# Performance work log

Measured on AMD Instinct MI355X. Metric: run time of the kernel, lower is better.

Reference implementation:

```python
import jax, jax.numpy as jnp
import numpy as np

N, C, H, W = 4, 128, 64, 64
HEADS, KS, RED = 4, 7, 18
D = C // HEADS


def _layernorm(x, w, b, eps=1e-5):
    mu = x.mean(axis=-1, keepdims=True)
    var = ((x - mu) ** 2).mean(axis=-1, keepdims=True)
    return (x - mu) * jax.lax.rsqrt(var + eps) * w + b


def _gelu(x):
    return jax.nn.gelu(x, approximate=False)


def setup_inputs() -> dict:
    key = jax.random.key(0)
    ks = jax.random.split(key, 16)
    s = 0.02
    inp = {
        'x': jax.random.normal(ks[0], (N, C, H, W), jnp.float32),
        'ln1_w': jnp.ones((C,), jnp.float32), 'ln1_b': jnp.zeros((C,), jnp.float32),
        'ln2_w': jnp.ones((C,), jnp.float32), 'ln2_b': jnp.zeros((C,), jnp.float32),
        'qkv_w': jax.random.normal(ks[1], (C, 3 * C), jnp.float32) * s,
        'qkv_b': jnp.zeros((3 * C,), jnp.float32),
        'proj_w': jax.random.normal(ks[2], (C, C), jnp.float32) * s,
        'proj_b': jnp.zeros((C,), jnp.float32),
        'rpb': jax.random.normal(ks[3], (HEADS, 2 * KS - 1, 2 * KS - 1), jnp.float32) * s,
        'conv1_w': jax.random.normal(ks[4], (C, C // 4), jnp.float32) * s,
        'conv1_b': jnp.zeros((C // 4,), jnp.float32),
        'conv2_w': jax.random.normal(ks[5], (C // 4, C), jnp.float32) * s,
        'conv2_b': jnp.zeros((C,), jnp.float32),
        'ca1_w': jax.random.normal(ks[6], (C, C // RED), jnp.float32) * s,
        'ca1_b': jnp.zeros((C // RED,), jnp.float32),
        'ca2_w': jax.random.normal(ks[7], (C // RED, C), jnp.float32) * s,
        'ca2_b': jnp.zeros((C,), jnp.float32),
        'fc1_w': jax.random.normal(ks[8], (C, 4 * C), jnp.float32) * s,
        'fc1_b': jnp.zeros((4 * C,), jnp.float32),
        'fc2_w': jax.random.normal(ks[9], (4 * C, C), jnp.float32) * s,
        'fc2_b': jnp.zeros((C,), jnp.float32),
    }
    return inp


def _na2d(xc, qkv_w, qkv_b, rpb, proj_w, proj_b):
    # xc: [N, H, W, C] -> neighborhood attention with clamped k x k windows (NATTEN semantics)
    n, h, w, c = xc.shape
    qkv = (xc @ qkv_w + qkv_b).reshape(n, h, w, 3, HEADS, D)
    q, k, v = qkv[..., 0, :, :], qkv[..., 1, :, :], qkv[..., 2, :, :]
    q = q * (D ** -0.5)
    half = KS // 2
    ni = jnp.clip(jnp.arange(h) - half, 0, h - KS)          # window start per query row
    nj = jnp.clip(jnp.arange(w) - half, 0, w - KS)
    idx_i = ni[:, None] + jnp.arange(KS)                     # [H, KS]
    idx_j = nj[:, None] + jnp.arange(KS)                     # [W, KS]
    # gather key/value windows: [N, H, KS, W, KS, heads, D]
    kw = k[:, idx_i][:, :, :, idx_j]
    vw = v[:, idx_i][:, :, :, idx_j]
    attn = jnp.einsum('nijhd,niajbhd->nijhab', q, kw)        # [N,H,W,heads,KS,KS]
    bi = idx_i - jnp.arange(h)[:, None] + (KS - 1)           # rel-pos bias row index [H,KS]
    bj = idx_j - jnp.arange(w)[:, None] + (KS - 1)           # [W,KS]
    bias = rpb[:, bi][:, :, :, bj]                           # [heads,H,KS,W,KS]
    attn = attn + bias.transpose(1, 3, 0, 2, 4)[None]        # -> [1,H,W,heads,KS,KS]
    attn = jax.nn.softmax(attn.reshape(n, h, w, HEADS, KS * KS), axis=-1)
    attn = attn.reshape(n, h, w, HEADS, KS, KS)
    out = jnp.einsum('nijhab,niajbhd->nijhd', attn, vw).reshape(n, h, w, c)
    return out @ proj_w + proj_b


def reference(x, ln1_w, ln1_b, ln2_w, ln2_b, qkv_w, qkv_b, proj_w, proj_b, rpb,
              conv1_w, conv1_b, conv2_w, conv2_b, ca1_w, ca1_b, ca2_w, ca2_b,
              fc1_w, fc1_b, fc2_w, fc2_b):
    n, c, h, w = x.shape
    xs = x.transpose(0, 2, 3, 1).reshape(n, h * w, c)        # n (h w) c
    shortcut = xs
    xn = _layernorm(xs, ln1_w, ln1_b)
    xc = xn.reshape(n, h, w, c)
    # conv branch: 1x1 -> GELU -> 1x1 -> channel attention
    t = _gelu(xc @ conv1_w + conv1_b) @ conv2_w + conv2_b
    g = t.mean(axis=(1, 2))                                  # global avg pool [N,C]
    g = jax.nn.sigmoid(jax.nn.relu(g @ ca1_w + ca1_b) @ ca2_w + ca2_b)
    ca_x = (t * g[:, None, None, :]).reshape(n, h * w, c)
    # neighborhood attention branch
    na_x = _na2d(xc, qkv_w, qkv_b, rpb, proj_w, proj_b).reshape(n, h * w, c)
    x2 = shortcut + na_x + ca_x * 0.02
    m = _gelu(_layernorm(x2, ln2_w, ln2_b) @ fc1_w + fc1_b) @ fc2_w + fc2_b
    x3 = x2 + m
    return x3.reshape(n, h, w, c).transpose(0, 3, 1, 2)
```

## Files before the change

kernel.cpp:

```cpp
#include <hip/hip_runtime.h>
#include <hip/hip_bf16.h>
#include <math.h>

#define NB 4
#define CC 128
#define HH 64
#define WW 64
#define HEADS 4
#define KS 7
#define DD 32
#define HW 4096
#define MTOT 16384

typedef unsigned short BF;
typedef short short8 __attribute__((ext_vector_type(8)));
typedef float floatx4 __attribute__((ext_vector_type(4)));

__device__ __forceinline__ float gelu_f(float x) {
    return 0.5f * x * (1.0f + erff(x * 0.70710678118654752440f));
}

__device__ __forceinline__ BF f2bf(float f) {
    union { float f; unsigned u; } a; a.f = f;
    unsigned u = a.u;
    unsigned r = u + 0x7FFFu + ((u >> 16) & 1u);
    return (BF)(r >> 16);
}

__device__ __forceinline__ float bf2f(BF v) {
    return __uint_as_float(((unsigned)v) << 16);
}

#define LDK 40
#define LDK128 136

__global__ __launch_bounds__(256) void ln1t_kernel(
    const float* __restrict__ x, const float* __restrict__ w,
    const float* __restrict__ b, BF* __restrict__ out,
    float* __restrict__ part,
    const float* __restrict__ qkv_w, const float* __restrict__ conv1_w,
    const float* __restrict__ conv2_w, const float* __restrict__ proj_w,
    const float* __restrict__ fc1_w, const float* __restrict__ fc2_w,
    BF* __restrict__ qkvT, BF* __restrict__ c1T, BF* __restrict__ c2T,
    BF* __restrict__ projT2, BF* __restrict__ fc1T2, BF* __restrict__ fc2T2)
{
    const int blk = blockIdx.x;
    const int t  = threadIdx.x;

    if (blk >= 512) {
        for (int idx = (blk - 512) * 256 + t; idx < 204800; idx += 32768) {
            if (idx < 49152) {
                int l = idx, n = l >> 7, k = l & 127;
                qkvT[l] = f2bf(qkv_w[k * 384 + n]);
            } else if (idx < 53248) {
                int l = idx - 49152, n = l >> 7, k = l & 127;
                c1T[l] = f2bf(conv1_w[k * 32 + n]);
            } else if (idx < 57344) {
                int l = idx - 53248, n = l >> 5, k = l & 31;
                c2T[l] = f2bf(conv2_w[k * 128 + n]);
            } else if (idx < 73728) {
                int l = idx - 57344, kk = l & 31, n = (l >> 5) & 127, ks = l >> 12;
                projT2[l] = f2bf(proj_w[(ks * 32 + kk) * 128 + n]);
            } else if (idx < 139264) {
                int l = idx - 73728, kk = l & 31, n = (l >> 5) & 511, ks = l >> 14;
                fc1T2[l] = f2bf(fc1_w[(ks * 32 + kk) * 512 + n]);
            } else {
                int l = idx - 139264, kk = l & 31, n = (l >> 5) & 127, ks = l >> 12;
                fc2T2[l] = f2bf(fc2_w[(ks * 32 + kk) * 128 + n]);
            }
        }
        return;
    }

    __shared__ float xt[128][33];
    __shared__ float mus[32], rss[32];
    const int n  = blk >> 7;
    const int p0 = (blk & 127) * 32;
    if (blk < 4 && t < 128) part[blk * CC + t] = 0.f;

    {
        int pp = t & 31, c8 = t >> 5;
        #pragma unroll 4
        for (int it = 0; it < 16; it++) {
            int c = it * 8 + c8;
            xt[c][pp] = x[(size_t)(n * CC + c) * HW + p0 + pp];
        }
    }
    __syncthreads();
    {
        int pp2 = t >> 3, cb = t & 7;
        float s = 0.f;
        #pragma unroll
        for (int u = 0; u < 16; u++) s += xt[cb + u * 8][pp2];
        s += __shfl_xor(s, 1); s += __shfl_xor(s, 2); s += __shfl_xor(s, 4);
        float mu = s * (1.0f / CC);
        float v = 0.f;
        #pragma unroll
        for (int u = 0; u < 16; u++) { float d = xt[cb + u * 8][pp2] - mu; v += d * d; }
        v += __shfl_xor(v, 1); v += __shfl_xor(v, 2); v += __shfl_xor(v, 4);
        if (cb == 0) { mus[pp2] = mu; rss[pp2] = rsqrtf(v * (1.0f / CC) + 1e-5f); }
    }
    __syncthreads();
    {
        #pragma unroll
        for (int it = 0; it < 2; it++) {
            int pp2 = (t >> 4) + it * 16;
            int c0  = (t & 15) * 8;
            float mu = mus[pp2], rs = rss[pp2];
            int m = n * HW + p0 + pp2;
            short8 o;
            #pragma unroll
            for (int u = 0; u < 8; u++)
                o[u] = (short)f2bf((xt[c0 + u][pp2] - mu) * rs * w[c0 + u] + b[c0 + u]);
            *(short8*)(out + (size_t)m * CC + c0) = o;
        }
    }
}

__global__ __launch_bounds__(256) void phase2(
    const BF* __restrict__ xn, const BF* __restrict__ qkvT,
    const float* __restrict__ qkv_b, BF* __restrict__ qkv_out,
    const BF* __restrict__ c1T, const float* __restrict__ b1,
    const BF* __restrict__ c2T, const float* __restrict__ b2,
    BF* __restrict__ tout, float* __restrict__ part)
{
    __shared__ __align__(16) char smem[26624];
    const int bid = blockIdx.x;
    const int t = threadIdx.x;
    const int w = t >> 6, lane = t & 63, q = lane >> 4, r16 = lane & 15;

    if (bid < 768) {
        BF* Bl = (BF*)smem;
        const int col0 = (bid % 6) * 64;
        const int row0 = (bid / 6) * 128;
        {
            int nn = t >> 2;
            int kk = (t & 3) * 32;
            const BF* src = qkvT + (size_t)(col0 + nn) * 128 + kk;
            #pragma unroll
            for (int u = 0; u < 4; u++)
                *(uint4*)(Bl + nn * LDK128 + kk + u * 8) = *(const uint4*)(src + u * 8);
        }
        __syncthreads();
        #pragma unroll
        for (int half = 0; half < 2; half++) {
            floatx4 acc[4] = {};
            const BF* arow = xn + (size_t)(row0 + half * 64 + w * 16 + r16) * CC;
            #pragma unroll
            for (int ks = 0; ks < 4; ks++) {
                short8 af = *(const short8*)(arow + ks * 32 + q * 8);
                #pragma unroll
                for (int nt = 0; nt < 4; nt++) {
                    short8 bf = *(const short8*)(Bl + (nt * 16 + r16) * LDK128 + ks * 32 + q * 8);
                    acc[nt] = __builtin_amdgcn_mfma_f32_16x16x32_bf16(af, bf, acc[nt], 0, 0, 0);
                }
            }
            #pragma unroll
            for (int nt = 0; nt < 4; nt++) {
                int col = col0 + nt * 16 + r16;
                float bv = qkv_b[col];
                #pragma unroll
                for (int reg = 0; reg < 4; reg++) {
                    int row = row0 + half * 64 + w * 16 + q * 4 + reg;
                    qkv_out[(size_t)row * 384 + col] = f2bf(acc[nt][reg] + bv);
                }
            }
        }
        return;
    }
    BF*    W1l = (BF*)smem;
    BF*    W2l = (BF*)(smem + 8704);
    BF*    Hl  = (BF*)(smem + 18944);
    float* red = (float*)(smem + 24064);
    const int row0 = (bid - 768) * 64;
    {
        #pragma unroll
        for (int it = 0; it < 2; it++) {
            int idx = it * 256 + t;
            int nn = idx >> 4, u = idx & 15;
            *(uint4*)(W1l + nn * LDK128 + u * 8) = *(const uint4*)(c1T + nn * 128 + u * 8);
        }
    }
    {
        #pragma unroll
        for (int it = 0; it < 2; it++) {
            int idx = it * 256 + t;
            int nn = idx >> 2, u = idx & 3;
            *(uint4*)(W2l + nn * LDK + u * 8) = *(const uint4*)(c2T + nn * 32 + u * 8);
        }
    }
    __syncthreads();
    floatx4 a1[2] = {};
    const BF* arow = xn + (size_t)(row0 + w * 16 + r16) * CC;
    #pragma unroll
    for (int ks = 0; ks < 4; ks++) {
        short8 af = *(const short8*)(arow + ks * 32 + q * 8);
        #pragma unroll
        for (int nt = 0; nt < 2; nt++) {
            short8 bf = *(const short8*)(W1l + (nt * 16 + r16) * LDK128 + ks * 32 + q * 8);
            a1[nt] = __builtin_amdgcn_mfma_f32_16x16x32_bf16(af, bf, a1[nt], 0, 0, 0);
        }
    }
    #pragma unroll
    for (int nt = 0; nt < 2; nt++) {
        int col = nt * 16 + r16;
        float bv = b1[col];
        #pragma unroll
        for (int reg = 0; reg < 4; reg++)
            Hl[(w * 16 + q * 4 + reg) * LDK + col] = f2bf(gelu_f(a1[nt][reg] + bv));
    }
    __syncthreads();
    floatx4 a2[8] = {};
    short8 af2 = *(const short8*)(Hl + (w * 16 + r16) * LDK + q * 8);
    #pragma unroll
    for (int nt = 0; nt < 8; nt++) {
        short8 bf = *(const short8*)(W2l + (nt * 16 + r16) * LDK + q * 8);
        a2[nt] = __builtin_amdgcn_mfma_f32_16x16x32_bf16(af2, bf, a2[nt], 0, 0, 0);
    }
    #pragma unroll
    for (int nt = 0; nt < 8; nt++) {
        int col = nt * 16 + r16;
        float bv = b2[col];
        float s = 0.f;
        #pragma unroll
        for (int reg = 0; reg < 4; reg++) {
            int row = row0 + w * 16 + q * 4 + reg;
            float v = a2[nt][reg] + bv;
            tout[(size_t)row * CC + col] = f2bf(v);
            s += v;
        }
        s += __shfl_xor(s, 16);
        s += __shfl_xor(s, 32);
        if (lane < 16) red[w * 128 + col] = s;
    }
    __syncthreads();
    if (t < 128) {
        float cs = red[t] + red[128 + t] + red[256 + t] + red[384 + t];
        atomicAdd(&part[(row0 >> 12) * CC + t], cs);
    }
}

__global__ __launch_bounds__(256) void na_mfma_kernel(
    const BF* __restrict__ qkv, const float* __restrict__ rpb,
    BF* __restrict__ outp)
{
    __shared__ __align__(16) BF Kt[224][40];
    __shared__ __align__(16) BF Vt[32][232];
    __shared__ __align__(16) BF Qb[64][40];
    __shared__ __align__(16) BF Pl[4][16][232];
    __shared__ float rb[169];

    const int b = blockIdx.x;
    const int h = b & 3;
    const int tile = b >> 2;
    const int n = tile >> 6;
    const int ti = (tile >> 3) & 7, tj = tile & 7;
    const int t = threadIdx.x;
    const int w = t >> 6, lane = t & 63, quad = lane >> 4, r16 = lane & 15;
    const int i0 = ti * 8, j0 = tj * 8;
    const int wi0 = max(i0 - 3, 0), wj0 = max(j0 - 3, 0);
    const int R  = min(wi0 + 13, 63) - wi0 + 1;
    const int Rj = min(wj0 + 13, 63) - wj0 + 1;

    for (int idx = t; idx < 896; idx += 256) {
        int key = idx >> 2, ch = idx & 3;
        int kr = key >> 4, kc = key & 15;
        uint4 v = {0u, 0u, 0u, 0u};
        if (kr < R && kc < Rj) {
            size_t pix = (size_t)((n * HH + wi0 + kr) * WW + wj0 + kc);
            v = *(const uint4*)(qkv + pix * 384 + 128 + h * DD + ch * 8);
        }
        *(uint4*)&Kt[key][ch * 8] = v;
    }
    for (int idx = t; idx < 896; idx += 256) {
        int key = idx >> 2, ch = idx & 3;
        int kr = key >> 4, kc = key & 15;
        if (kr < R && kc < Rj) {
            size_t pix = (size_t)((n * HH + wi0 + kr) * WW + wj0 + kc);
            uint4 v = *(const uint4*)(qkv + pix * 384 + 256 + h * DD + ch * 8);
            const BF* pv = (const BF*)&v;
            #pragma unroll
            for (int u = 0; u < 8; u++) Vt[ch * 8 + u][key] = pv[u];
        } else {
            #pragma unroll
            for (int u = 0; u < 8; u++) Vt[ch * 8 + u][key] = 0;
        }
    }
    {
        int q = t >> 2, ch = t & 3;
        size_t mq = (size_t)((n * HH + i0 + (q >> 3)) * WW + j0 + (q & 7));
        *(uint4*)&Qb[q][ch * 8] = *(const uint4*)(qkv + mq * 384 + h * DD + ch * 8);
    }
    if (t < 169) rb[t] = rpb[h * 169 + t];
    __syncthreads();

    const int kt0 = min(max(i0 + 2 * w - 3, 0), HH - KS) - wi0;

    int oi[4], cok[4], bj0[4], ai_[4];
    #pragma unroll
    for (int reg = 0; reg < 4; reg++) {
        int q = w * 16 + quad * 4 + reg;
        int i = i0 + (q >> 3), j = j0 + (q & 7);
        int ni = min(max(i - 3, 0), HH - KS), nj = min(max(j - 3, 0), WW - KS);
        oi[reg]  = ni - wi0;
        ai_[reg] = ni - i + 6;
        int dc = r16 - (nj - wj0);
        cok[reg] = ((unsigned)dc < 7u) ? 1 : 0;
        bj0[reg] = min(max(dc + (nj - j + 6), 0), 12);
    }

    short8 aq = *(const short8*)&Qb[w * 16 + r16][quad * 8];
    floatx4 S[8];
    #pragma unroll
    for (int jt = 0; jt < 8; jt++) {
        floatx4 z = {0.f, 0.f, 0.f, 0.f};
        short8 bk = *(const short8*)&Kt[(kt0 + jt) * 16 + r16][quad * 8];
        S[jt] = __builtin_amdgcn_mfma_f32_16x16x32_bf16(aq, bk, z, 0, 0, 0);
    }
    const float scale = 0.17677669529663688110f;
    #pragma unroll
    for (int jt = 0; jt < 8; jt++) {
        #pragma unroll
        for (int reg = 0; reg < 4; reg++) {
            int dr = kt0 + jt - oi[reg];
            bool ok = ((unsigned)dr < 7u) && cok[reg];
            int bi = min(max(dr + ai_[reg], 0), 12);
            float bias = rb[bi * 13 + bj0[reg]];
            S[jt][reg] = ok ? fmaf(S[jt][reg], scale, bias) : -1e30f;
        }
    }
    float rinv[4];
    #pragma unroll
    for (int reg = 0; reg < 4; reg++) {
        float m = S[0][reg];
        #pragma unroll
        for (int jt = 1; jt < 8; jt++) m = fmaxf(m, S[jt][reg]);
        m = fmaxf(m, __shfl_xor(m, 1));
        m = fmaxf(m, __shfl_xor(m, 2));
        m = fmaxf(m, __shfl_xor(m, 4));
        m = fmaxf(m, __shfl_xor(m, 8));
        float s = 0.f;
        #pragma unroll
        for (int jt = 0; jt < 8; jt++) {
            float e = __expf(S[jt][reg] - m);
            S[jt][reg] = e;
            s += e;
        }
        s += __shfl_xor(s, 1);
        s += __shfl_xor(s, 2);
        s += __shfl_xor(s, 4);
        s += __shfl_xor(s, 8);
        rinv[reg] = 1.0f / s;
    }
    #pragma unroll
    for (int jt = 0; jt < 8; jt++)
        #pragma unroll
        for (int reg = 0; reg < 4; reg++)
            Pl[w][quad * 4 + reg][(kt0 + jt) * 16 + r16] = f2bf(S[jt][reg] * rinv[reg]);
    if (kt0 & 1) {
        #pragma unroll
        for (int reg = 0; reg < 4; reg++) {
            Pl[w][quad * 4 + reg][(kt0 - 1) * 16 + r16] = 0;
            Pl[w][quad * 4 + reg][(kt0 + 8) * 16 + r16] = 0;
        }
    }

    const int ks0 = kt0 >> 1;
    const int nch = 4 + (kt0 & 1);
    floatx4 O0 = {0.f, 0.f, 0.f, 0.f}, O1 = {0.f, 0.f, 0.f, 0.f};
    #pragma unroll
    for (int c2 = 0; c2 < 5; c2++) {
        if (c2 < nch) {
            int ks = ks0 + c2;
            short8 ap = *(const short8*)&Pl[w][r16][ks * 32 + quad * 8];
            short8 b0 = *(const short8*)&Vt[r16][ks * 32 + quad * 8];
            short8 b1 = *(const short8*)&Vt[16 + r16][ks * 32 + quad * 8];
            O0 = __builtin_amdgcn_mfma_f32_16x16x32_bf16(ap, b0, O0, 0, 0, 0);
            O1 = __builtin_amdgcn_mfma_f32_16x16x32_bf16(ap, b1, O1, 0, 0, 0);
        }
    }
    #pragma unroll
    for (int reg = 0; reg < 4; reg++) {
        int q = w * 16 + quad * 4 + reg;
        size_t m = (size_t)((n * HH + i0 + (q >> 3)) * WW + j0 + (q & 7));
        outp[m * CC + h * DD + r16]      = f2bf(O0[reg]);
        outp[m * CC + h * DD + 16 + r16] = f2bf(O1[reg]);
    }
}

__global__ __launch_bounds__(256) void tail_kernel(
    const BF* __restrict__ A, const BF* __restrict__ projT2,
    const float* __restrict__ proj_b, const float* __restrict__ x,
    const BF* __restrict__ tbuf, const float* __restrict__ part,
    const float* __restrict__ ca1_w, const float* __restrict__ ca1_b,
    const float* __restrict__ ca2_w, const float* __restrict__ ca2_b,
    const float* __restrict__ w2, const float* __restrict__ b2,
    const BF* __restrict__ fc1T2, const float* __restrict__ fc1_b,
    const BF* __restrict__ fc2T2, const float* __restrict__ fc2_b,
    float* __restrict__ out)
{
    __shared__ __align__(16) char sarena[9216];
    __shared__ __align__(16) BF ln2l[16][136];
    __shared__ __align__(16) BF hl[16][520];
    __shared__ float gs[128], h1s[8], gl[128];
    __shared__ float S1[4][16], S2[4][16];

    float* xs = (float*)sarena;
    float* st = (float*)sarena;

    const int t = threadIdx.x;
    const int w = t >> 6, lane = t & 63, quad = lane >> 4, r16 = lane & 15;
    const int row0 = blockIdx.x * 16;
    const int n = row0 >> 12, p0 = row0 & 4095;

    #pragma unroll
    for (int it = 0; it < 2; it++) {
        int idx4 = it * 256 + t;
        int p4 = idx4 & 3, c = idx4 >> 2;
        float4 v = *(const float4*)(x + (size_t)(n * CC + c) * HW + p0 + p4 * 4);
        xs[(p4 * 4 + 0) * 132 + c] = v.x; xs[(p4 * 4 + 1) * 132 + c] = v.y;
        xs[(p4 * 4 + 2) * 132 + c] = v.z; xs[(p4 * 4 + 3) * 132 + c] = v.w;
    }
    if (t < 128) gs[t] = part[n * CC + t] * (1.0f / HW);
    __syncthreads();
    if (t < 7) {
        float a = ca1_b[t];
        for (int k = 0; k < 128; k++) a += gs[k] * ca1_w[k * 7 + t];
        h1s[t] = fmaxf(a, 0.f);
    }
    __syncthreads();
    if (t < 128) {
        float o = ca2_b[t];
        #pragma unroll
        for (int r = 0; r < 7; r++) o += h1s[r] * ca2_w[r * 128 + t];
        gl[t] = 1.0f / (1.0f + expf(-o));
    }

    floatx4 acc[2] = {};
    const BF* arow = A + (size_t)(row0 + r16) * CC;
    #pragma unroll
    for (int ks = 0; ks < 4; ks++) {
        short8 af = *(const short8*)(arow + ks * 32 + quad * 8);
        #pragma unroll
        for (int nt = 0; nt < 2; nt++) {
            int col = w * 32 + nt * 16 + r16;
            short8 bf = *(const short8*)(projT2 + ((size_t)(ks * 128 + col)) * 32 + quad * 8);
            acc[nt] = __builtin_amdgcn_mfma_f32_16x16x32_bf16(af, bf, acc[nt], 0, 0, 0);
        }
    }
    __syncthreads();

    float x2r[2][4];
    float s1[4] = {0.f, 0.f, 0.f, 0.f}, s2[4] = {0.f, 0.f, 0.f, 0.f};
    #pragma unroll
    for (int nt = 0; nt < 2; nt++) {
        int col = w * 32 + nt * 16 + r16;
        float bv = proj_b[col], gv = gl[col];
        #pragma unroll
        for (int reg = 0; reg < 4; reg++) {
            int lr = quad * 4 + reg;
            float tv = bf2f(tbuf[(size_t)(row0 + lr) * CC + col]);
            float v = acc[nt][reg] + bv + xs[lr * 132 + col] + 0.02f * tv * gv;
            x2r[nt][reg] = v;
            s1[reg] += v; s2[reg] += v * v;
        }
    }
    #pragma unroll
    for (int reg = 0; reg < 4; reg++) {
        #pragma unroll
        for (int off = 1; off < 16; off <<= 1) {
            s1[reg] += __shfl_xor(s1[reg], off);
            s2[reg] += __shfl_xor(s2[reg], off);
        }
    }
    if (r16 == 0) {
        #pragma unroll
        for (int reg = 0; reg < 4; reg++) {
            S1[w][quad * 4 + reg] = s1[reg];
            S2[w][quad * 4 + reg] = s2[reg];
        }
    }
    __syncthreads();
    float mu[4], rr[4];
    #pragma unroll
    for (int reg = 0; reg < 4; reg++) {
        int r = quad * 4 + reg;
        float t1 = S1[0][r] + S1[1][r] + S1[2][r] + S1[3][r];
        float t2 = S2[0][r] + S2[1][r] + S2[2][r] + S2[3][r];
        mu[reg] = t1 * (1.0f / CC);
        float var = t2 * (1.0f / CC) - mu[reg] * mu[reg];
        rr[reg] = rsqrtf(var + 1e-5f);
    }
    #pragma unroll
    for (int nt = 0; nt < 2; nt++) {
        int col = w * 32 + nt * 16 + r16;
        float wv = w2[col], bv2 = b2[col];
        #pragma unroll
        for (int reg = 0; reg < 4; reg++) {
            int lr = quad * 4 + reg;
            ln2l[lr][col] = f2bf((x2r[nt][reg] - mu[reg]) * rr[reg] * wv + bv2);
        }
    }
    __syncthreads();

    short8 af1[4];
    #pragma unroll
    for (int ks = 0; ks < 4; ks++)
        af1[ks] = *(const short8*)&ln2l[r16][ks * 32 + quad * 8];
    floatx4 a2[8] = {};
    #pragma unroll
    for (int ks = 0; ks < 4; ks++) {
        #pragma unroll
        for (int nt = 0; nt < 8; nt++) {
            int col = w * 128 + nt * 16 + r16;
            short8 bf = *(const short8*)(fc1T2 + ((size_t)(ks * 512 + col)) * 32 + quad * 8);
            a2[nt] = __builtin_amdgcn_mfma_f32_16x16x32_bf16(af1[ks], bf, a2[nt], 0, 0, 0);
        }
    }
    #pragma unroll
    for (int nt = 0; nt < 8; nt++) {
        int col = w * 128 + nt * 16 + r16;
        float bv = fc1_b[col];
        #pragma unroll
        for (int reg = 0; reg < 4; reg++) {
            int lr = quad * 4 + reg;
            hl[lr][col] = f2bf(gelu_f(a2[nt][reg] + bv));
        }
    }
    __syncthreads();

    floatx4 a3[2] = {};
    #pragma unroll
    for (int ks = 0; ks < 16; ks++) {
        short8 af = *(const short8*)&hl[r16][ks * 32 + quad * 8];
        #pragma unroll
        for (int nt = 0; nt < 2; nt++) {
            int col = w * 32 + nt * 16 + r16;
            short8 bf = *(const short8*)(fc2T2 + ((size_t)(ks * 128 + col)) * 32 + quad * 8);
            a3[nt] = __builtin_amdgcn_mfma_f32_16x16x32_bf16(af, bf, a3[nt], 0, 0, 0);
        }
    }
    __syncthreads();
    #pragma unroll
    for (int nt = 0; nt < 2; nt++) {
        int col = w * 32 + nt * 16 + r16;
        float bv = fc2_b[col];
        #pragma unroll
        for (int reg = 0; reg < 4; reg++) {
            int lr = quad * 4 + reg;
            st[col * 18 + lr] = a3[nt][reg] + bv + x2r[nt][reg];
        }
    }
    __syncthreads();
    {
        int col = t >> 1, half = t & 1;
        float* dst = out + (size_t)(n * CC + col) * HW + p0 + half * 8;
        #pragma unroll
        for (int u = 0; u < 2; u++) {
            float4 v;
            v.x = st[col * 18 + half * 8 + u * 4 + 0];
            v.y = st[col * 18 + half * 8 + u * 4 + 1];
            v.z = st[col * 18 + half * 8 + u * 4 + 2];
            v.w = st[col * 18 + half * 8 + u * 4 + 3];
            *(float4*)(dst + u * 4) = v;
        }
    }
}

extern "C" void kernel_launch(void* const* d_in, const int* in_sizes, int n_in,
                              void* d_out, int out_size, void* d_ws, size_t ws_size,
                              hipStream_t stream)
{
    const float* x       = (const float*)d_in[0];
    const float* ln1_w   = (const float*)d_in[1];
    const float* ln1_b   = (const float*)d_in[2];
    const float* ln2_w   = (const float*)d_in[3];
    const float* ln2_b   = (const float*)d_in[4];
    const float* qkv_w   = (const float*)d_in[5];
    const float* qkv_b   = (const float*)d_in[6];
    const float* proj_w  = (const float*)d_in[7];
    const float* proj_b  = (const float*)d_in[8];
    const float* rpb     = (const float*)d_in[9];
    const float* conv1_w = (const float*)d_in[10];
    const float* conv1_b = (const float*)d_in[11];
    const float* conv2_w = (const float*)d_in[12];
    const float* conv2_b = (const float*)d_in[13];
    const float* ca1_w   = (const float*)d_in[14];
    const float* ca1_b   = (const float*)d_in[15];
    const float* ca2_w   = (const float*)d_in[16];
    const float* ca2_b   = (const float*)d_in[17];
    const float* fc1_w   = (const float*)d_in[18];
    const float* fc1_b   = (const float*)d_in[19];
    const float* fc2_w   = (const float*)d_in[20];
    const float* fc2_b   = (const float*)d_in[21];
    float* out = (float*)d_out;

    char* ws = (char*)d_ws;
    BF*    xn_bf   = (BF*)(ws);
    BF*    qkv_bf  = (BF*)(ws + 4194304);
    BF*    t_bf    = (BF*)(ws + 16777216);
    BF*    na_bf   = (BF*)(ws + 20971520);
    float* part    = (float*)(ws + 25165824);
    BF*    qkvT    = (BF*)(ws + 25167872);
    BF*    c1T     = (BF*)(ws + 25266176);
    BF*    c2T     = (BF*)(ws + 25274368);
    BF*    projT2  = (BF*)(ws + 25282560);
    BF*    fc1T2   = (BF*)(ws + 25315328);
    BF*    fc2T2   = (BF*)(ws + 25446400);

    ln1t_kernel<<<640, 256, 0, stream>>>(x, ln1_w, ln1_b, xn_bf, part,
        qkv_w, conv1_w, conv2_w, proj_w, fc1_w, fc2_w,
        qkvT, c1T, c2T, projT2, fc1T2, fc2T2);
    phase2<<<1024, 256, 0, stream>>>(xn_bf, qkvT, qkv_b, qkv_bf,
                                     c1T, conv1_b, c2T, conv2_b, t_bf, part);
    na_mfma_kernel<<<1024, 256, 0, stream>>>(qkv_bf, rpb, na_bf);
    tail_kernel<<<1024, 256, 0, stream>>>(na_bf, projT2, proj_b, x, t_bf, part,
                                          ca1_w, ca1_b, ca2_w, ca2_b,
                                          ln2_w, ln2_b, fc1T2, fc1_b,
                                          fc2T2, fc2_b, out);
}
```

Before: 164.7 us.

## Hoist channel-attention gate into NA kernel and double tail rows per block

```diff
diff --git a/kernel.cpp b/kernel.cpp
--- a/kernel.cpp
+++ b/kernel.cpp
@@ -242,7 +242,11 @@
 
 __global__ __launch_bounds__(256) void na_mfma_kernel(
     const BF* __restrict__ qkv, const float* __restrict__ rpb,
-    BF* __restrict__ outp)
+    BF* __restrict__ outp,
+    const float* __restrict__ part,
+    const float* __restrict__ ca1_w, const float* __restrict__ ca1_b,
+    const float* __restrict__ ca2_w, const float* __restrict__ ca2_b,
+    float* __restrict__ glw)
 {
     __shared__ __align__(16) BF Kt[224][40];
     __shared__ __align__(16) BF Vt[32][232];
@@ -251,11 +255,44 @@
     __shared__ float rb[169];
 
     const int b = blockIdx.x;
+    const int t = threadIdx.x;
+
+    if (b == 1024) {
+        float* gsm = (float*)Kt;
+        float* h1s = (float*)Qb;
+        if (t < 128) {
+            #pragma unroll
+            for (int nn = 0; nn < 4; nn++)
+                gsm[nn * 128 + t] = part[nn * CC + t] * (1.0f / HW);
+        }
+        __syncthreads();
+        if (t < 224) {
+            int pair = t >> 3, s = t & 7;
+            int nn = pair / 7, r = pair % 7;
+            float a = 0.f;
+            #pragma unroll
+            for (int k = 0; k < 16; k++)
+                a += gsm[nn * 128 + s + k * 8] * ca1_w[(s + k * 8) * 7 + r];
+            a += __shfl_xor(a, 1); a += __shfl_xor(a, 2); a += __shfl_xor(a, 4);
+            if (s == 0) h1s[pair] = fmaxf(a + ca1_b[r], 0.f);
+        }
+        __syncthreads();
+        if (t < 128) {
+            #pragma unroll
+            for (int nn = 0; nn < 4; nn++) {
+                float o = ca2_b[t];
+                #pragma unroll
+                for (int r = 0; r < 7; r++) o += h1s[nn * 7 + r] * ca2_w[r * 128 + t];
+                glw[nn * CC + t] = 1.0f / (1.0f + expf(-o));
+            }
+        }
+        return;
+    }
+
     const int h = b & 3;
     const int tile = b >> 2;
     const int n = tile >> 6;
     const int ti = (tile >> 3) & 7, tj = tile & 7;
-    const int t = threadIdx.x;
     const int w = t >> 6, lane = t & 63, quad = lane >> 4, r16 = lane & 15;
     const int i0 = ti * 8, j0 = tj * 8;
     const int wi0 = max(i0 - 3, 0), wj0 = max(j0 - 3, 0);
@@ -388,180 +425,192 @@
     }
 }
 
-__global__ __launch_bounds__(256) void tail_kernel(
+__global__ __launch_bounds__(256, 2) void tail_kernel(
     const BF* __restrict__ A, const BF* __restrict__ projT2,
     const float* __restrict__ proj_b, const float* __restrict__ x,
-    const BF* __restrict__ tbuf, const float* __restrict__ part,
-    const float* __restrict__ ca1_w, const float* __restrict__ ca1_b,
-    const float* __restrict__ ca2_w, const float* __restrict__ ca2_b,
+    const BF* __restrict__ tbuf, const float* __restrict__ glw,
     const float* __restrict__ w2, const float* __restrict__ b2,
     const BF* __restrict__ fc1T2, const float* __restrict__ fc1_b,
     const BF* __restrict__ fc2T2, const float* __restrict__ fc2_b,
     float* __restrict__ out)
 {
-    __shared__ __align__(16) char sarena[9216];
-    __shared__ __align__(16) BF ln2l[16][136];
-    __shared__ __align__(16) BF hl[16][520];
-    __shared__ float gs[128], h1s[8], gl[128];
-    __shared__ float S1[4][16], S2[4][16];
+    __shared__ __align__(16) char sarena[17408];
+    __shared__ __align__(16) BF ln2l[32][136];
+    __shared__ __align__(16) BF hl[32][520];
+    __shared__ float gl[128];
+    __shared__ float S1[2][4][16], S2[2][4][16];
 
     float* xs = (float*)sarena;
     float* st = (float*)sarena;
 
     const int t = threadIdx.x;
     const int w = t >> 6, lane = t & 63, quad = lane >> 4, r16 = lane & 15;
-    const int row0 = blockIdx.x * 16;
+    const int row0 = blockIdx.x * 32;
     const int n = row0 >> 12, p0 = row0 & 4095;
 
     #pragma unroll
-    for (int it = 0; it < 2; it++) {
+    for (int it = 0; it < 4; it++) {
         int idx4 = it * 256 + t;
-        int p4 = idx4 & 3, c = idx4 >> 2;
+        int p4 = idx4 & 7, c = idx4 >> 3;
         float4 v = *(const float4*)(x + (size_t)(n * CC + c) * HW + p0 + p4 * 4);
         xs[(p4 * 4 + 0) * 132 + c] = v.x; xs[(p4 * 4 + 1) * 132 + c] = v.y;
         xs[(p4 * 4 + 2) * 132 + c] = v.z; xs[(p4 * 4 + 3) * 132 + c] = v.w;
     }
-    if (t < 128) gs[t] = part[n * CC + t] * (1.0f / HW);
-    __syncthreads();
-    if (t < 7) {
-        float a = ca1_b[t];
-        for (int k = 0; k < 128; k++) a += gs[k] * ca1_w[k * 7 + t];
-        h1s[t] = fmaxf(a, 0.f);
-    }
-    __syncthreads();
-    if (t < 128) {
-        float o = ca2_b[t];
-        #pragma unroll
-        for (int r = 0; r < 7; r++) o += h1s[r] * ca2_w[r * 128 + t];
-        gl[t] = 1.0f / (1.0f + expf(-o));
-    }
-
-    floatx4 acc[2] = {};
-    const BF* arow = A + (size_t)(row0 + r16) * CC;
+    if (t < 128) gl[t] = glw[n * CC + t];
+
+    floatx4 acc[2][2] = {};
+    const BF* ar0 = A + (size_t)(row0 + r16) * CC;
+    const BF* ar1 = A + (size_t)(row0 + 16 + r16) * CC;
     #pragma unroll
     for (int ks = 0; ks < 4; ks++) {
-        short8 af = *(const short8*)(arow + ks * 32 + quad * 8);
+        short8 a0 = *(const short8*)(ar0 + ks * 32 + quad * 8);
+        short8 a1 = *(const short8*)(ar1 + ks * 32 + quad * 8);
         #pragma unroll
         for (int nt = 0; nt < 2; nt++) {
             int col = w * 32 + nt * 16 + r16;
             short8 bf = *(const short8*)(projT2 + ((size_t)(ks * 128 + col)) * 32 + quad * 8);
-            acc[nt] = __builtin_amdgcn_mfma_f32_16x16x32_bf16(af, bf, acc[nt], 0, 0, 0);
-        }
-    }
-    __syncthreads();
-
-    float x2r[2][4];
-    float s1[4] = {0.f, 0.f, 0.f, 0.f}, s2[4] = {0.f, 0.f, 0.f, 0.f};
-    #pragma unroll
-    for (int nt = 0; nt < 2; nt++) {
-        int col = w * 32 + nt * 16 + r16;
-        float bv = proj_b[col], gv = gl[col];
+            acc[0][nt] = __builtin_amdgcn_mfma_f32_16x16x32_bf16(a0, bf, acc[0][nt], 0, 0, 0);
+            acc[1][nt] = __builtin_amdgcn_mfma_f32_16x16x32_bf16(a1, bf, acc[1][nt], 0, 0, 0);
+        }
+    }
+    __syncthreads();
+
+    float x2r[2][2][4];
+    float s1[2][4] = {}, s2[2][4] = {};
+    #pragma unroll
+    for (int tile = 0; tile < 2; tile++) {
+        #pragma unroll
+        for (int nt = 0; nt < 2; nt++) {
+            int col = w * 32 + nt * 16 + r16;
+            float bv = proj_b[col], gv = gl[col];
+            #pragma unroll
+            for (int reg = 0; reg < 4; reg++) {
+                int lr = tile * 16 + quad * 4 + reg;
+                float tv = bf2f(tbuf[(size_t)(row0 + lr) * CC + col]);
+                float v = acc[tile][nt][reg] + bv + xs[lr * 132 + col] + 0.02f * tv * gv;
+                x2r[tile][nt][reg] = v;
+                s1[tile][reg] += v; s2[tile][reg] += v * v;
+            }
+        }
+    }
+    #pragma unroll
+    for (int tile = 0; tile < 2; tile++) {
         #pragma unroll
         for (int reg = 0; reg < 4; reg++) {
-            int lr = quad * 4 + reg;
-            float tv = bf2f(tbuf[(size_t)(row0 + lr) * CC + col]);
-            float v = acc[nt][reg] + bv + xs[lr * 132 + col] + 0.02f * tv * gv;
-            x2r[nt][reg] = v;
-            s1[reg] += v; s2[reg] += v * v;
-        }
-    }
-    #pragma unroll
-    for (int reg = 0; reg < 4; reg++) {
-        #pragma unroll
-        for (int off = 1; off < 16; off <<= 1) {
-            s1[reg] += __shfl_xor(s1[reg], off);
-            s2[reg] += __shfl_xor(s2[reg], off);
+            #pragma unroll
+            for (int off = 1; off < 16; off <<= 1) {
+                s1[tile][reg] += __shfl_xor(s1[tile][reg], off);
+                s2[tile][reg] += __shfl_xor(s2[tile][reg], off);
+            }
         }
     }
     if (r16 == 0) {
         #pragma unroll
+        for (int tile = 0; tile < 2; tile++)
+            #pragma unroll
+            for (int reg = 0; reg < 4; reg++) {
+                S1[tile][w][quad * 4 + reg] = s1[tile][reg];
+                S2[tile][w][quad * 4 + reg] = s2[tile][reg];
+            }
+    }
+    __syncthreads();
+    float mu[2][4], rr[2][4];
+    #pragma unroll
+    for (int tile = 0; tile < 2; tile++) {
+        #pragma unroll
         for (int reg = 0; reg < 4; reg++) {
-            S1[w][quad * 4 + reg] = s1[reg];
-            S2[w][quad * 4 + reg] = s2[reg];
-        }
-    }
-    __syncthreads();
-    float mu[4], rr[4];
-    #pragma unroll
-    for (int reg = 0; reg < 4; reg++) {
-        int r = quad * 4 + reg;
-        float t1 = S1[0][r] + S1[1][r] + S1[2][r] + S1[3][r];
-        float t2 = S2[0][r] + S2[1][r] + S2[2][r] + S2[3][r];
-        mu[reg] = t1 * (1.0f / CC);
-        float var = t2 * (1.0f / CC) - mu[reg] * mu[reg];
-        rr[reg] = rsqrtf(var + 1e-5f);
-    }
-    #pragma unroll
-    for (int nt = 0; nt < 2; nt++) {
-        int col = w * 32 + nt * 16 + r16;
-        float wv = w2[col], bv2 = b2[col];
-        #pragma unroll
-        for (int reg = 0; reg < 4; reg++) {
-            int lr = quad * 4 + reg;
-            ln2l[lr][col] = f2bf((x2r[nt][reg] - mu[reg]) * rr[reg] * wv + bv2);
-        }
-    }
-    __syncthreads();
-
-    short8 af1[4];
-    #pragma unroll
-    for (int ks = 0; ks < 4; ks++)
-        af1[ks] = *(const short8*)&ln2l[r16][ks * 32 + quad * 8];
-    floatx4 a2[8] = {};
+            int r = quad * 4 + reg;
+            float t1 = S1[tile][0][r] + S1[tile][1][r] + S1[tile][2][r] + S1[tile][3][r];
+            float t2 = S2[tile][0][r] + S2[tile][1][r] + S2[tile][2][r] + S2[tile][3][r];
+            mu[tile][reg] = t1 * (1.0f / CC);
+            float var = t2 * (1.0f / CC) - mu[tile][reg] * mu[tile][reg];
+            rr[tile][reg] = rsqrtf(var + 1e-5f);
+        }
+    }
+    #pragma unroll
+    for (int tile = 0; tile < 2; tile++) {
+        #pragma unroll
+        for (int nt = 0; nt < 2; nt++) {
+            int col = w * 32 + nt * 16 + r16;
+            float wv = w2[col], bv2 = b2[col];
+            #pragma unroll
+            for (int reg = 0; reg < 4; reg++) {
+                int lr = tile * 16 + quad * 4 + reg;
+                ln2l[lr][col] = f2bf((x2r[tile][nt][reg] - mu[tile][reg]) * rr[tile][reg] * wv + bv2);
+            }
+        }
+    }
+    __syncthreads();
+
+    short8 af1[2][4];
+    #pragma unroll
+    for (int tile = 0; tile < 2; tile++)
+        #pragma unroll
+        for (int ks = 0; ks < 4; ks++)
+            af1[tile][ks] = *(const short8*)&ln2l[tile * 16 + r16][ks * 32 + quad * 8];
+    floatx4 c1[2][8] = {};
     #pragma unroll
     for (int ks = 0; ks < 4; ks++) {
         #pragma unroll
         for (int nt = 0; nt < 8; nt++) {
             int col = w * 128 + nt * 16 + r16;
             short8 bf = *(const short8*)(fc1T2 + ((size_t)(ks * 512 + col)) * 32 + quad * 8);
-            a2[nt] = __builtin_amdgcn_mfma_f32_16x16x32_bf16(af1[ks], bf, a2[nt], 0, 0, 0);
-        }
-    }
-    #pragma unroll
-    for (int nt = 0; nt < 8; nt++) {
-        int col = w * 128 + nt * 16 + r16;
-        float bv = fc1_b[col];
-        #pragma unroll
-        for (int reg = 0; reg < 4; reg++) {
-            int lr = quad * 4 + reg;
-            hl[lr][col] = f2bf(gelu_f(a2[nt][reg] + bv));
-        }
-    }
-    __syncthreads();
-
-    floatx4 a3[2] = {};
+            c1[0][nt] = __builtin_amdgcn_mfma_f32_16x16x32_bf16(af1[0][ks], bf, c1[0][nt], 0, 0, 0);
+            c1[1][nt] = __builtin_amdgcn_mfma_f32_16x16x32_bf16(af1[1][ks], bf, c1[1][nt], 0, 0, 0);
+        }
+    }
+    #pragma unroll
+    for (int tile = 0; tile < 2; tile++) {
+        #pragma unroll
+        for (int nt = 0; nt < 8; nt++) {
+            int col = w * 128 + nt * 16 + r16;
+            float bv = fc1_b[col];
+            #pragma unroll
+            for (int reg = 0; reg < 4; reg++) {
+                int lr = tile * 16 + quad * 4 + reg;
+                hl[lr][col] = f2bf(gelu_f(c1[tile][nt][reg] + bv));
+            }
+        }
+    }
+    __syncthreads();
+
+    floatx4 c2[2][2] = {};
     #pragma unroll
     for (int ks = 0; ks < 16; ks++) {
-        short8 af = *(const short8*)&hl[r16][ks * 32 + quad * 8];
+        short8 h0 = *(const short8*)&hl[r16][ks * 32 + quad * 8];
+        short8 h1 = *(const short8*)&hl[16 + r16][ks * 32 + quad * 8];
         #pragma unroll
         for (int nt = 0; nt < 2; nt++) {
             int col = w * 32 + nt * 16 + r16;
             short8 bf = *(const short8*)(fc2T2 + ((size_t)(ks * 128 + col)) * 32 + quad * 8);
-            a3[nt] = __builtin_amdgcn_mfma_f32_16x16x32_bf16(af, bf, a3[nt], 0, 0, 0);
-        }
-    }
-    __syncthreads();
-    #pragma unroll
-    for (int nt = 0; nt < 2; nt++) {
-        int col = w * 32 + nt * 16 + r16;
-        float bv = fc2_b[col];
-        #pragma unroll
-        for (int reg = 0; reg < 4; reg++) {
-            int lr = quad * 4 + reg;
-            st[col * 18 + lr] = a3[nt][reg] + bv + x2r[nt][reg];
+            c2[0][nt] = __builtin_amdgcn_mfma_f32_16x16x32_bf16(h0, bf, c2[0][nt], 0, 0, 0);
+            c2[1][nt] = __builtin_amdgcn_mfma_f32_16x16x32_bf16(h1, bf, c2[1][nt], 0, 0, 0);
+        }
+    }
+    #pragma unroll
+    for (int tile = 0; tile < 2; tile++) {
+        #pragma unroll
+        for (int nt = 0; nt < 2; nt++) {
+            int col = w * 32 + nt * 16 + r16;
+            float bv = fc2_b[col];
+            #pragma unroll
+            for (int reg = 0; reg < 4; reg++) {
+                int lr = tile * 16 + quad * 4 + reg;
+                st[col * 34 + lr] = c2[tile][nt][reg] + bv + x2r[tile][nt][reg];
+            }
         }
     }
     __syncthreads();
     {
         int col = t >> 1, half = t & 1;
-        float* dst = out + (size_t)(n * CC + col) * HW + p0 + half * 8;
-        #pragma unroll
-        for (int u = 0; u < 2; u++) {
+        float* dst = out + (size_t)(n * CC + col) * HW + p0 + half * 16;
+        #pragma unroll
+        for (int u = 0; u < 4; u++) {
             float4 v;
-            v.x = st[col * 18 + half * 8 + u * 4 + 0];
-            v.y = st[col * 18 + half * 8 + u * 4 + 1];
-            v.z = st[col * 18 + half * 8 + u * 4 + 2];
-            v.w = st[col * 18 + half * 8 + u * 4 + 3];
+            v.x = st[col * 34 + half * 16 + u * 4 + 0];
+            v.y = st[col * 34 + half * 16 + u * 4 + 1];
+            v.z = st[col * 34 + half * 16 + u * 4 + 2];
+            v.w = st[col * 34 + half * 16 + u * 4 + 3];
             *(float4*)(dst + u * 4) = v;
         }
     }
@@ -607,15 +656,16 @@
     BF*    projT2  = (BF*)(ws + 25282560);
     BF*    fc1T2   = (BF*)(ws + 25315328);
     BF*    fc2T2   = (BF*)(ws + 25446400);
+    float* glw     = (float*)(ws + 25577472);
 
     ln1t_kernel<<<640, 256, 0, stream>>>(x, ln1_w, ln1_b, xn_bf, part,
         qkv_w, conv1_w, conv2_w, proj_w, fc1_w, fc2_w,
         qkvT, c1T, c2T, projT2, fc1T2, fc2T2);
     phase2<<<1024, 256, 0, stream>>>(xn_bf, qkvT, qkv_b, qkv_bf,
                                      c1T, conv1_b, c2T, conv2_b, t_bf, part);
-    na_mfma_kernel<<<1024, 256, 0, stream>>>(qkv_bf, rpb, na_bf);
-    tail_kernel<<<1024, 256, 0, stream>>>(na_bf, projT2, proj_b, x, t_bf, part,
-                                          ca1_w, ca1_b, ca2_w, ca2_b,
-                                          ln2_w, ln2_b, fc1T2, fc1_b,
-                                          fc2T2, fc2_b, out);
-}
+    na_mfma_kernel<<<1025, 256, 0, stream>>>(qkv_bf, rpb, na_bf,
+                                             part, ca1_w, ca1_b, ca2_w, ca2_b, glw);
+    tail_kernel<<<512, 256, 0, stream>>>(na_bf, projT2, proj_b, x, t_bf, glw,
+                                         ln2_w, ln2_b, fc1T2, fc1_b,
+                                         fc2T2, fc2_b, out);
+}
```

Result: faster. 158.6 us (-3.7%).
